# Optimization experiments

Hardware: AMD Instinct MI355X
Metric: run time of the kernel (lower is better)

The kernel has to match this reference:

```python
import jax, jax.numpy as jnp
import numpy as np

MAX_NORM = 1.0
B, V, C, VOCAB, E = 256, 50, 32, 100000, 128


def setup_inputs() -> dict:
    key = jax.random.key(0)
    k1, k2, k3 = jax.random.split(key, 3)
    W = jax.random.normal(k1, (VOCAB, E), dtype=jnp.float32)
    codes = jax.random.randint(k2, (B, V, C), 0, VOCAB, dtype=jnp.int64)
    n_visits = jax.random.randint(k3, (B,), 1, V + 1, dtype=jnp.int64)
    # ensure batch_max_visits == V (static output shape, matches min(max(len), max_visits))
    n_visits = n_visits.at[0].set(V)
    return {"W": W, "codes": codes, "n_visits": n_visits}


def reference(W, codes, n_visits):
    # Faithful to the torch module: expand_visits produces offsets [0,1,...,nv-1],
    # so EmbeddingBag('sum') bag i = emb(flat[i]) for i < nv-1, and the last bag
    # sums emb(flat[nv-1 : nv*C]). Result is top-padded to V rows per patient.
    b, v, c = codes.shape
    L = v * c
    flat = codes.reshape(b, L)                     # flattened codes per patient
    g = W[flat]                                    # [B, L, E] gathered rows
    # EmbeddingBag max_norm: renormalize looked-up rows whose norm exceeds MAX_NORM
    norms = jnp.linalg.norm(g, axis=-1, keepdims=True)
    g = g * jnp.minimum(1.0, MAX_NORM / jnp.maximum(norms, 1e-12))
    # prefix sums: cs0[:, j] = sum of g[:, :j]
    cs0 = jnp.concatenate([jnp.zeros((b, 1, g.shape[-1]), g.dtype),
                           jnp.cumsum(g, axis=1)], axis=1)  # [B, L+1, E]
    nv = n_visits.astype(jnp.int32)                # [B]
    end = (nv * c)[:, None, None]                  # sum over real flattened codes
    start = (nv - 1)[:, None, None]
    S = (jnp.take_along_axis(cs0, end, axis=1)
         - jnp.take_along_axis(cs0, start, axis=1))  # [B, 1, E] last-bag sum
    r = jnp.arange(v, dtype=jnp.int32)[None, :]    # output row index
    i = r - (v - nv[:, None])                      # bag index (negative => pad row)
    ei = jnp.take_along_axis(g, jnp.clip(i, 0, L - 1)[:, :, None], axis=1)  # [B, V, E]
    out = jnp.where((i >= 0)[:, :, None],
                    jnp.where((i < nv[:, None] - 1)[:, :, None], ei, S),
                    jnp.zeros_like(ei))
    return out
```

## Files before the change

kernel.cpp:

```cpp
#include <hip/hip_runtime.h>
#include <math.h>

#define B_     256
#define V_     50
#define C_     32
#define E_     128
#define VOCAB_ 100000
#define L_     (V_ * C_)
#define SPB    8
#define NCHUNK (SPB * 4)
#define NBLK   (B_ * SPB)

__global__ __launch_bounds__(256, 6) void fused_kernel(
    const float* __restrict__ W,
    const int*   __restrict__ codes,
    const int*   __restrict__ nvis,
    float*       __restrict__ out,
    float*       __restrict__ part)
{
    const int tid  = threadIdx.x;
    const int wave = tid >> 6;
    const int lane = tid & 63;
    const int g    = lane >> 4;
    const int l4   = lane & 15;

    const int b  = blockIdx.x >> 3;
    const int s  = blockIdx.x & (SPB - 1);
    const int nv = nvis[b];
    const int* cf = codes + b * L_;
    float* ob = out + (size_t)b * V_ * E_;

    {
        const int i = (wave * 4 + g) * SPB + s;
        if (i < V_ - 1) {
            if (i < nv - 1) {
                const int code = cf[i];
                const float* row = W + (size_t)code * E_;
                float4 v1 = ((const float4*)row)[l4];
                float4 v2 = ((const float4*)row)[16 + l4];
                float ss = v1.x*v1.x + v1.y*v1.y + v1.z*v1.z + v1.w*v1.w
                         + v2.x*v2.x + v2.y*v2.y + v2.z*v2.z + v2.w*v2.w;
                #pragma unroll
                for (int m = 1; m <= 8; m <<= 1) ss += __shfl_xor(ss, m, 64);
                const float sc = fminf(1.0f, 1.0f / fmaxf(sqrtf(ss), 1e-12f));
                float* orow = ob + (size_t)(V_ - nv + i) * E_;
                ((float4*)orow)[l4]      = make_float4(v1.x*sc, v1.y*sc, v1.z*sc, v1.w*sc);
                ((float4*)orow)[16 + l4] = make_float4(v2.x*sc, v2.y*sc, v2.z*sc, v2.w*sc);
            } else {
                float* orow = ob + (size_t)(i - (nv - 1)) * E_;
                ((float4*)orow)[l4]      = make_float4(0.f, 0.f, 0.f, 0.f);
                ((float4*)orow)[16 + l4] = make_float4(0.f, 0.f, 0.f, 0.f);
            }
        }
    }

    const int j0    = nv - 1;
    const int j1    = nv * C_;
    const int chunk = (j1 - j0 + NCHUNK - 1) / NCHUNK;
    const int wid   = s * 4 + wave;
    const int a0    = j0 + wid * chunk;
    const int n     = min(a0 + chunk, j1) - a0;

    int cl = 0;
    if (lane < n) cl = cf[a0 + lane];

    float4 a1 = make_float4(0.f, 0.f, 0.f, 0.f);
    float4 a2 = make_float4(0.f, 0.f, 0.f, 0.f);
    #pragma unroll 4
    for (int t = 0; t < n; t += 4) {
        const int tt   = t + g;
        const int code = __shfl(cl, tt, 64);
        const float* row = W + (size_t)code * E_;
        float4 v1 = ((const float4*)row)[l4];
        float4 v2 = ((const float4*)row)[16 + l4];
        float ss = v1.x*v1.x + v1.y*v1.y + v1.z*v1.z + v1.w*v1.w
                 + v2.x*v2.x + v2.y*v2.y + v2.z*v2.z + v2.w*v2.w;
        #pragma unroll
        for (int m = 1; m <= 8; m <<= 1) ss += __shfl_xor(ss, m, 64);
        float sc = fminf(1.0f, 1.0f / fmaxf(sqrtf(ss), 1e-12f));
        if (tt >= n) sc = 0.0f;
        a1.x += v1.x*sc; a1.y += v1.y*sc; a1.z += v1.z*sc; a1.w += v1.w*sc;
        a2.x += v2.x*sc; a2.y += v2.y*sc; a2.z += v2.z*sc; a2.w += v2.w*sc;
    }

    #pragma unroll
    for (int m = 16; m <= 32; m <<= 1) {
        a1.x += __shfl_xor(a1.x, m, 64); a1.y += __shfl_xor(a1.y, m, 64);
        a1.z += __shfl_xor(a1.z, m, 64); a1.w += __shfl_xor(a1.w, m, 64);
        a2.x += __shfl_xor(a2.x, m, 64); a2.y += __shfl_xor(a2.y, m, 64);
        a2.z += __shfl_xor(a2.z, m, 64); a2.w += __shfl_xor(a2.w, m, 64);
    }

    __shared__ float4 s1[4][16], s2[4][16];
    if (lane < 16) { s1[wave][l4] = a1; s2[wave][l4] = a2; }
    __syncthreads();
    if (tid < 32) {
        const int h = tid >> 4;
        const int q = tid & 15;
        float4 f = (h == 0) ? s1[0][q] : s2[0][q];
        #pragma unroll
        for (int w = 1; w < 4; w++) {
            float4 p = (h == 0) ? s1[w][q] : s2[w][q];
            f.x += p.x; f.y += p.y; f.z += p.z; f.w += p.w;
        }
        ((float4*)(part + (size_t)blockIdx.x * E_))[tid] = f;
    }
}

__global__ __launch_bounds__(128) void reduce_kernel(
    const float* __restrict__ part,
    float*       __restrict__ out)
{
    const int b = blockIdx.x;
    const int t = threadIdx.x;
    const float* p = part + (size_t)b * SPB * E_;
    float acc = 0.0f;
    #pragma unroll
    for (int s = 0; s < SPB; s++) acc += p[s * E_ + t];
    out[((size_t)b * V_ + (V_ - 1)) * E_ + t] = acc;
}

extern "C" void kernel_launch(void* const* d_in, const int* in_sizes, int n_in,
                              void* d_out, int out_size, void* d_ws, size_t ws_size,
                              hipStream_t stream) {
    const float* W     = (const float*)d_in[0];
    const int*   codes = (const int*)d_in[1];
    const int*   nvis  = (const int*)d_in[2];
    float*       out   = (float*)d_out;
    float*       part  = (float*)d_ws;

    fused_kernel<<<NBLK, 256, 0, stream>>>(W, codes, nvis, out, part);
    reduce_kernel<<<B_, 128, 0, stream>>>(part, out);
}
```

Before: 97.80 us.

## Precompute per-row renorm scales for whole vocabulary in separate kernel

Adds a pre-pass kernel that computes the max-norm scale for every vocabulary row and stores it in workspace. The gather kernels then look up that scale instead of doing a per-lookup sum of squares and shuffle reduction. This drops the ALU and shuffle work in the hot loop. In exchange, the pre-pass reads the whole 51 MB table every call, which is far more traffic than the roughly 200K gathered rows (about 100 MB with repeats), and it adds a launch.

After: 106.1 us. 8.5% more time.

```diff
diff --git a/kernel.cpp b/kernel.cpp
--- a/kernel.cpp
+++ b/kernel.cpp
@@ -11,10 +11,37 @@
 #define NCHUNK (SPB * 4)
 #define NBLK   (B_ * SPB)
 
+#define NROWS_PER_BLK 16
+#define NORM_BLKS (VOCAB_ / NROWS_PER_BLK)
+#define PART_OFF_BYTES (1 << 19)
+
+
+__global__ __launch_bounds__(256) void norm_kernel(
+    const float* __restrict__ W,
+    float*       __restrict__ nscale)
+{
+    const int tid  = threadIdx.x;
+    const int wave = tid >> 6;
+    const int lane = tid & 63;
+    const int g    = lane >> 4;
+    const int l4   = lane & 15;
+    const int row  = blockIdx.x * NROWS_PER_BLK + wave * 4 + g;
+    const float4* r = (const float4*)(W + (size_t)row * E_);
+    float4 v1 = r[l4];
+    float4 v2 = r[16 + l4];
+    float ss = v1.x*v1.x + v1.y*v1.y + v1.z*v1.z + v1.w*v1.w
+             + v2.x*v2.x + v2.y*v2.y + v2.z*v2.z + v2.w*v2.w;
+    #pragma unroll
+    for (int m = 1; m <= 8; m <<= 1) ss += __shfl_xor(ss, m, 64);
+    if (l4 == 0)
+        nscale[row] = fminf(1.0f, 1.0f / fmaxf(sqrtf(ss), 1e-12f));
+}
+
 __global__ __launch_bounds__(256, 6) void fused_kernel(
     const float* __restrict__ W,
     const int*   __restrict__ codes,
     const int*   __restrict__ nvis,
+    const float* __restrict__ nscale,
     float*       __restrict__ out,
     float*       __restrict__ part)
 {
@@ -30,6 +57,15 @@
     const int* cf = codes + b * L_;
     float* ob = out + (size_t)b * V_ * E_;
 
+    const int j0    = nv - 1;
+    const int j1    = nv * C_;
+    const int chunk = (j1 - j0 + NCHUNK - 1) / NCHUNK;
+    const int wid   = s * 4 + wave;
+    const int a0    = j0 + wid * chunk;
+    const int n     = min(a0 + chunk, j1) - a0;
+    int cl = 0;
+    if (lane < n) cl = cf[a0 + lane];
+
     {
         const int i = (wave * 4 + g) * SPB + s;
         if (i < V_ - 1) {
@@ -38,11 +74,7 @@
                 const float* row = W + (size_t)code * E_;
                 float4 v1 = ((const float4*)row)[l4];
                 float4 v2 = ((const float4*)row)[16 + l4];
-                float ss = v1.x*v1.x + v1.y*v1.y + v1.z*v1.z + v1.w*v1.w
-                         + v2.x*v2.x + v2.y*v2.y + v2.z*v2.z + v2.w*v2.w;
-                #pragma unroll
-                for (int m = 1; m <= 8; m <<= 1) ss += __shfl_xor(ss, m, 64);
-                const float sc = fminf(1.0f, 1.0f / fmaxf(sqrtf(ss), 1e-12f));
+                const float sc = nscale[code];
                 float* orow = ob + (size_t)(V_ - nv + i) * E_;
                 ((float4*)orow)[l4]      = make_float4(v1.x*sc, v1.y*sc, v1.z*sc, v1.w*sc);
                 ((float4*)orow)[16 + l4] = make_float4(v2.x*sc, v2.y*sc, v2.z*sc, v2.w*sc);
@@ -54,15 +86,8 @@
         }
     }
 
-    const int j0    = nv - 1;
-    const int j1    = nv * C_;
-    const int chunk = (j1 - j0 + NCHUNK - 1) / NCHUNK;
-    const int wid   = s * 4 + wave;
-    const int a0    = j0 + wid * chunk;
-    const int n     = min(a0 + chunk, j1) - a0;
-
-    int cl = 0;
-    if (lane < n) cl = cf[a0 + lane];
+    float sl = 0.0f;
+    if (lane < n) sl = nscale[cl];
 
     float4 a1 = make_float4(0.f, 0.f, 0.f, 0.f);
     float4 a2 = make_float4(0.f, 0.f, 0.f, 0.f);
@@ -70,15 +95,11 @@
     for (int t = 0; t < n; t += 4) {
         const int tt   = t + g;
         const int code = __shfl(cl, tt, 64);
+        float sc       = __shfl(sl, tt, 64);
+        if (tt >= n) sc = 0.0f;
         const float* row = W + (size_t)code * E_;
         float4 v1 = ((const float4*)row)[l4];
         float4 v2 = ((const float4*)row)[16 + l4];
-        float ss = v1.x*v1.x + v1.y*v1.y + v1.z*v1.z + v1.w*v1.w
-                 + v2.x*v2.x + v2.y*v2.y + v2.z*v2.z + v2.w*v2.w;
-        #pragma unroll
-        for (int m = 1; m <= 8; m <<= 1) ss += __shfl_xor(ss, m, 64);
-        float sc = fminf(1.0f, 1.0f / fmaxf(sqrtf(ss), 1e-12f));
-        if (tt >= n) sc = 0.0f;
         a1.x += v1.x*sc; a1.y += v1.y*sc; a1.z += v1.z*sc; a1.w += v1.w*sc;
         a2.x += v2.x*sc; a2.y += v2.y*sc; a2.z += v2.z*sc; a2.w += v2.w*sc;
     }
@@ -127,8 +148,10 @@
     const int*   codes = (const int*)d_in[1];
     const int*   nvis  = (const int*)d_in[2];
     float*       out   = (float*)d_out;
-    float*       part  = (float*)d_ws;
+    float*       nscale = (float*)d_ws;
+    float*       part   = (float*)((char*)d_ws + PART_OFF_BYTES);
 
-    fused_kernel<<<NBLK, 256, 0, stream>>>(W, codes, nvis, out, part);
+    norm_kernel<<<NORM_BLKS, 256, 0, stream>>>(W, nscale);
+    fused_kernel<<<NBLK, 256, 0, stream>>>(W, codes, nvis, nscale, out, part);
     reduce_kernel<<<B_, 128, 0, stream>>>(part, out);
 }
```
